# Kernel optimization log

Hardware: AMD Instinct MI355X
Metric: run time of the kernel (lower is better)

The kernel has to match this reference:

```python
import jax, jax.numpy as jnp
import numpy as np

N_NODES = 50000
N_EDGES = 1_600_000
IN_CH = 128
HIDDEN = 64
OUT_CH = 1


def glorot(key, shape):
    limit = np.sqrt(6.0 / (shape[0] + shape[1]))
    return jax.random.uniform(key, shape, jnp.float32, -limit, limit)


def setup_inputs() -> dict:
    key = jax.random.key(0)
    ks = jax.random.split(key, 6)
    x = jax.random.normal(ks[0], (N_NODES, IN_CH), jnp.float32)
    edge_index = jax.random.randint(ks[1], (2, N_EDGES), 0, N_NODES, jnp.int64)
    W1 = glorot(ks[2], (IN_CH, HIDDEN))
    b1 = jnp.zeros((HIDDEN,), jnp.float32)
    W2 = glorot(ks[3], (HIDDEN, HIDDEN // 2))
    b2 = jnp.zeros((HIDDEN // 2,), jnp.float32)
    Wh = glorot(ks[4], (HIDDEN // 2, OUT_CH))
    bh = jnp.zeros((OUT_CH,), jnp.float32)
    return {"x": x, "edge_index": edge_index, "W1": W1, "b1": b1,
            "W2": W2, "b2": b2, "Wh": Wh, "bh": bh}


def gcn_conv(x, src, dst, W, b):
    """PyG-style GCNConv: H' = D^{-1/2} (A + I) D^{-1/2} X W + b."""
    n = x.shape[0]
    h = x @ W  # transform first (smaller message dim)
    # degree of A + I (all edge weights = 1, self-loop weight = 1)
    deg = jax.ops.segment_sum(jnp.ones(src.shape[0], h.dtype), dst,
                              num_segments=n) + 1.0
    dinv = deg ** -0.5
    norm = dinv[src] * dinv[dst]                      # [E]
    msg = h[src] * norm[:, None]                      # [E, F] gather
    agg = jax.ops.segment_sum(msg, dst, num_segments=n)  # scatter-add
    agg = agg + h * (dinv * dinv)[:, None]            # self-loop term
    return agg + b


def reference(x, edge_index, W1, b1, W2, b2, Wh, bh):
    src, dst = edge_index[0], edge_index[1]
    h = jax.nn.relu(gcn_conv(x, src, dst, W1, b1))
    # dropout: inference mode (training=False) -> identity
    h = jax.nn.relu(gcn_conv(h, src, dst, W2, b2))
    return h @ Wh + bh
```

## Files before the change

kernel.cpp:

```cpp
#include <hip/hip_runtime.h>

#define N_NODES 50000
#define IN_CH 128
#define HID 64
#define HID2 32

constexpr int NB = 391;
constexpr int CHUNK = 4096;
constexpr int CAP = 5120;
#define FPSCALE 524288.0f
#define FPINV   0x1p-19f
#define T1SCALE 2048.0f
#define T1INV   0x1p-11f

__device__ __forceinline__ unsigned short f2bf(float f) {
    union { float f; unsigned u; } v; v.f = f;
    unsigned r = v.u + 0x7fff + ((v.u >> 16) & 1);
    return (unsigned short)(r >> 16);
}
__device__ __forceinline__ float bflo(unsigned d) {
    union { unsigned u; float f; } v; v.u = d << 16; return v.f;
}
__device__ __forceinline__ float bfhi(unsigned d) {
    union { unsigned u; float f; } v; v.u = d & 0xffff0000u; return v.f;
}
__device__ __forceinline__ unsigned pack16(int a, int b) {
    return ((unsigned)a & 0xffffu) | ((unsigned)b << 16);
}
__device__ __forceinline__ void acc2(int& a0, int& a1, unsigned u) {
    a0 += (int)(short)(u & 0xffffu);
    a1 += ((int)u) >> 16;
}

__global__ __launch_bounds__(1024) void bin_kernel(const int* __restrict__ src,
                                                   const int* __restrict__ dst,
                                                   int* __restrict__ bcur,
                                                   unsigned short* __restrict__ psrc,
                                                   unsigned char* __restrict__ pbyte, int E) {
    __shared__ int hist[NB], lbase[NB], gbase[NB], lcur[NB];
    __shared__ unsigned outp[CHUNK];
    __shared__ int wsum[16];
    int tid = threadIdx.x, lane = tid & 63;
    int base = blockIdx.x * CHUNK;
    int cnt = min(CHUNK, E - base);
    for (int i = tid; i < NB; i += 1024) hist[i] = 0;
    int es[CHUNK / 1024], ed[CHUNK / 1024];
    __syncthreads();
#pragma unroll
    for (int k = 0; k < CHUNK / 1024; k++) {
        int e = base + k * 1024 + tid;
        if (e < E) {
            es[k] = src[e];
            ed[k] = dst[e];
            atomicAdd(&hist[ed[k] >> 7], 1);
        }
    }
    __syncthreads();
    {
        int v = (tid < NB) ? hist[tid] : 0;
        int s = v;
#pragma unroll
        for (int d = 1; d < 64; d <<= 1) {
            int t = __shfl_up(s, d, 64);
            if (lane >= d) s += t;
        }
        if (lane == 63 && tid < 512) wsum[tid >> 6] = s;
        __syncthreads();
        if (tid == 0) {
            int run = 0;
#pragma unroll
            for (int w = 0; w < 8; w++) { int t = wsum[w]; wsum[w] = run; run += t; }
        }
        __syncthreads();
        if (tid < NB) lbase[tid] = wsum[tid >> 6] + s - v;
    }
    __syncthreads();
    for (int i = tid; i < NB; i += 1024) {
        gbase[i] = i * CAP + (hist[i] ? atomicAdd(&bcur[i], hist[i]) : 0);
        lcur[i] = lbase[i];
    }
    __syncthreads();
#pragma unroll
    for (int k = 0; k < CHUNK / 1024; k++) {
        int e = base + k * 1024 + tid;
        if (e < E) {
            int b = ed[k] >> 7;
            int p = atomicAdd(&lcur[b], 1);
            outp[p] = ((unsigned)es[k] << 16) | (unsigned)ed[k];
        }
    }
    __syncthreads();
#pragma unroll
    for (int k = 0; k < CHUNK / 1024; k++) {
        int i = k * 1024 + tid;
        if (i < cnt) {
            unsigned p = outp[i];
            int d = (int)(p & 0xffffu);
            int b = d >> 7;
            int gp = gbase[b] + (i - lbase[b]);
            psrc[gp] = (unsigned short)(p >> 16);
            pbyte[gp] = (unsigned char)(d & 127);
        }
    }
}

__global__ __launch_bounds__(1024) void fine_kernel(unsigned short* __restrict__ psrc,
                                                    const unsigned char* __restrict__ pbyte,
                                                    const int* __restrict__ bcur,
                                                    int* __restrict__ off,
                                                    unsigned short* __restrict__ len,
                                                    float* __restrict__ dinv, int N) {
    __shared__ unsigned short lsrc[CAP];
    __shared__ unsigned char lb[CAP];
    __shared__ int fh[128], fb[128], fc[128];
    __shared__ int wsum2[2];
    int b = blockIdx.x, tid = threadIdx.x, lane = tid & 63;
    int gb = b * CAP;
    int cnt = min(bcur[b], CAP);
    if (tid < 128) fh[tid] = 0;
    __syncthreads();
    for (int i = tid; i < cnt; i += 1024) {
        lsrc[i] = psrc[gb + i];
        int dl = pbyte[gb + i];
        lb[i] = (unsigned char)dl;
        atomicAdd(&fh[dl], 1);
    }
    __syncthreads();
    {
        int v = (tid < 128) ? fh[tid] : 0;
        int s = v;
#pragma unroll
        for (int d = 1; d < 64; d <<= 1) {
            int t = __shfl_up(s, d, 64);
            if (lane >= d) s += t;
        }
        if (lane == 63 && tid < 128) wsum2[tid >> 6] = s;
        __syncthreads();
        if (tid < 128) fb[tid] = ((tid >> 6) ? wsum2[0] : 0) + s - v;
    }
    __syncthreads();
    if (tid < 128) {
        fc[tid] = fb[tid];
        int node = (b << 7) + tid;
        if (node < N) {
            off[node] = gb + fb[tid];
            len[node] = (unsigned short)fh[tid];
            dinv[node] = rsqrtf((float)fh[tid] + 1.0f);
        }
    }
    __syncthreads();
    for (int i = tid; i < cnt; i += 1024) {
        int p = atomicAdd(&fc[lb[i]], 1);
        psrc[gb + p] = lsrc[i];
    }
}

template <int K, int J, int NPB>
__global__ __launch_bounds__(256) void gemm_s_kernel(const float* __restrict__ X,
                                                     const float* __restrict__ W,
                                                     const float* __restrict__ dinv,
                                                     short* __restrict__ out, int N) {
    constexpr int QJ = J / 4;
    constexpr int NPT = NPB / (256 / QJ);
    static_assert(NPT == 2, "layout assumes 2 nodes/thread");
    constexpr int RG = K / 4;
    constexpr int RS = K + 4;
    __shared__ float Ws[K * J];
    __shared__ float Xs[NPB * RS];
    int tid = threadIdx.x;
    if (blockIdx.x == 0 && tid < J / 2)
        ((unsigned*)(out + (size_t)N * J))[tid] = 0;
    for (int i = tid; i < K * J / 4; i += 256) ((float4*)Ws)[i] = ((const float4*)W)[i];
    int n0 = blockIdx.x * NPB;
    for (int i = tid; i < NPB * RG; i += 256) {
        int r = i / RG, c = i % RG;
        int n = n0 + r;
        float4 v = make_float4(0.f, 0.f, 0.f, 0.f);
        if (n < N) v = ((const float4*)(X + (size_t)n * K))[c];
        *(float4*)&Xs[r * RS + ((c ^ (r & 7)) << 2)] = v;
    }
    __syncthreads();
    int q = tid % QJ, g = (tid / QJ) * NPT;
    const float* xr0 = &Xs[g * RS];
    const float* xr1 = &Xs[(g + 1) * RS];
    int sw0 = g & 7, sw1 = (g + 1) & 7;
    float4 a0 = make_float4(0.f, 0.f, 0.f, 0.f);
    float4 a1 = make_float4(0.f, 0.f, 0.f, 0.f);
#pragma unroll 8
    for (int k = 0; k < K; k++) {
        float4 w = *(const float4*)&Ws[k * J + q * 4];
        float x0 = xr0[(((k >> 2) ^ sw0) << 2) + (k & 3)];
        float x1 = xr1[(((k >> 2) ^ sw1) << 2) + (k & 3)];
        a0.x += x0 * w.x; a0.y += x0 * w.y; a0.z += x0 * w.z; a0.w += x0 * w.w;
        a1.x += x1 * w.x; a1.y += x1 * w.y; a1.z += x1 * w.z; a1.w += x1 * w.w;
    }
#pragma unroll
    for (int t = 0; t < NPT; t++) {
        int n = n0 + g + t;
        if (n < N) {
            float4 a = t ? a1 : a0;
            float d0 = dinv[n] * T1SCALE;
            int v0 = max(-32767, min(32767, (int)lrintf(a.x * d0)));
            int v1 = max(-32767, min(32767, (int)lrintf(a.y * d0)));
            int v2 = max(-32767, min(32767, (int)lrintf(a.z * d0)));
            int v3 = max(-32767, min(32767, (int)lrintf(a.w * d0)));
            *(uint2*)(out + (size_t)n * J + q * 4) = make_uint2(pack16(v0, v1), pack16(v2, v3));
        }
    }
}

__global__ __launch_bounds__(256) void agg1_fused_kernel(const unsigned short* __restrict__ sorted_src,
                                                         const int* __restrict__ off,
                                                         const unsigned short* __restrict__ len,
                                                         const float* __restrict__ dinv,
                                                         const short* __restrict__ xtab,
                                                         const float* __restrict__ b1,
                                                         const float* __restrict__ W2,
                                                         unsigned short* __restrict__ hws, int N) {
    __shared__ float hrow[4][HID];
    int tid = threadIdx.x, wid = tid >> 6, lane = tid & 63;
    if (blockIdx.x == 0 && tid < HID2 / 2)
        ((unsigned*)(hws + (size_t)N * HID2))[tid] = 0;
    int n = blockIdx.x * 4 + wid;
    if (n >= N) return;
    int g = lane >> 3, fl = lane & 7;
    int start = off[n], len_ = len[n];
    float dvn = dinv[n];
    const unsigned* tb = (const unsigned*)xtab;
    const unsigned char* tbb = (const unsigned char*)xtab;
    int acc[8] = {0, 0, 0, 0, 0, 0, 0, 0};
    if (len_ <= 64) {
        int sall = (lane < len_) ? (int)sorted_src[start + lane] : N;
        unsigned fo = ((unsigned)fl) << 4;
        int nit = (len_ + 31) >> 5;
        for (int t = 0; t < nit; t++) {
            int eb = (t << 5) + g;
            int s0 = __shfl(sall, eb, 64);
            int s1 = __shfl(sall, eb + 8, 64);
            int s2 = __shfl(sall, eb + 16, 64);
            int s3 = __shfl(sall, eb + 24, 64);
            uint4 q0 = *(const uint4*)(tbb + ((((unsigned)s0) << 7) + fo));
            uint4 q1 = *(const uint4*)(tbb + ((((unsigned)s1) << 7) + fo));
            uint4 q2 = *(const uint4*)(tbb + ((((unsigned)s2) << 7) + fo));
            uint4 q3 = *(const uint4*)(tbb + ((((unsigned)s3) << 7) + fo));
            acc2(acc[0], acc[1], q0.x); acc2(acc[2], acc[3], q0.y);
            acc2(acc[4], acc[5], q0.z); acc2(acc[6], acc[7], q0.w);
            acc2(acc[0], acc[1], q1.x); acc2(acc[2], acc[3], q1.y);
            acc2(acc[4], acc[5], q1.z); acc2(acc[6], acc[7], q1.w);
            acc2(acc[0], acc[1], q2.x); acc2(acc[2], acc[3], q2.y);
            acc2(acc[4], acc[5], q2.z); acc2(acc[6], acc[7], q2.w);
            acc2(acc[0], acc[1], q3.x); acc2(acc[2], acc[3], q3.y);
            acc2(acc[4], acc[5], q3.z); acc2(acc[6], acc[7], q3.w);
        }
    } else {
        int i = start + g, end = start + len_;
        for (; i < end; i += 8) {
            int s = sorted_src[i];
            uint4 q = *(const uint4*)(tb + (size_t)s * 32 + fl * 4);
            acc2(acc[0], acc[1], q.x); acc2(acc[2], acc[3], q.y);
            acc2(acc[4], acc[5], q.z); acc2(acc[6], acc[7], q.w);
        }
    }
#pragma unroll
    for (int m = 8; m <= 32; m <<= 1)
#pragma unroll
        for (int j = 0; j < 8; j++) acc[j] += __shfl_xor(acc[j], m, 64);
    if (g == 0) {
        float dis = dvn * T1INV;
        uint4 q = *(const uint4*)(tb + (size_t)n * 32 + fl * 4);
        int sv[8];
        sv[0] = (int)(short)(q.x & 0xffffu); sv[1] = ((int)q.x) >> 16;
        sv[2] = (int)(short)(q.y & 0xffffu); sv[3] = ((int)q.y) >> 16;
        sv[4] = (int)(short)(q.z & 0xffffu); sv[5] = ((int)q.z) >> 16;
        sv[6] = (int)(short)(q.w & 0xffffu); sv[7] = ((int)q.w) >> 16;
        float4 bb0 = *(const float4*)(b1 + fl * 8);
        float4 bb1 = *(const float4*)(b1 + fl * 8 + 4);
        float bbv[8] = {bb0.x, bb0.y, bb0.z, bb0.w, bb1.x, bb1.y, bb1.z, bb1.w};
        float o[8];
#pragma unroll
        for (int j = 0; j < 8; j++)
            o[j] = fmaxf((float)(acc[j] + sv[j]) * dis + bbv[j], 0.f);
        *(float4*)&hrow[wid][fl * 8]     = make_float4(o[0], o[1], o[2], o[3]);
        *(float4*)&hrow[wid][fl * 8 + 4] = make_float4(o[4], o[5], o[6], o[7]);
    }
    int j = lane & 31, half = lane >> 5;
    const float* hb = &hrow[wid][half << 5];
    const float* w2b = W2 + ((half << 5) * HID2) + j;
    float p = 0.f;
#pragma unroll
    for (int k4 = 0; k4 < 8; k4++) {
        float4 h4 = *(const float4*)(hb + (k4 << 2));
        p += h4.x * w2b[(k4 * 4 + 0) * HID2];
        p += h4.y * w2b[(k4 * 4 + 1) * HID2];
        p += h4.z * w2b[(k4 * 4 + 2) * HID2];
        p += h4.w * w2b[(k4 * 4 + 3) * HID2];
    }
    p += __shfl_xor(p, 32, 64);
    if (lane < 32)
        hws[(size_t)n * HID2 + j] = f2bf(p * dvn * FPSCALE);
}

__global__ __launch_bounds__(256) void agg2_final_kernel(const unsigned short* __restrict__ sorted_src,
                                                         const int* __restrict__ off,
                                                         const unsigned short* __restrict__ len,
                                                         const float* __restrict__ dinv,
                                                         const unsigned short* __restrict__ hws,
                                                         const float* __restrict__ b2,
                                                         const float* __restrict__ Wh,
                                                         const float* __restrict__ bh,
                                                         float* __restrict__ out, int N) {
    int lane = threadIdx.x & 63;
    int n = blockIdx.x * 4 + (threadIdx.x >> 6);
    if (n >= N) return;
    int g = lane >> 2, fl = lane & 3;
    int start = off[n], len_ = len[n];
    const unsigned char* hbb = (const unsigned char*)hws;
    int acc[8] = {0, 0, 0, 0, 0, 0, 0, 0};
    if (len_ <= 64) {
        int sall = (lane < len_) ? (int)sorted_src[start + lane] : N;
        unsigned fo = ((unsigned)fl) << 4;
        int s0 = __shfl(sall, g, 64);
        int s1 = __shfl(sall, g + 16, 64);
        int s2 = __shfl(sall, g + 32, 64);
        int s3 = __shfl(sall, g + 48, 64);
        uint4 q0 = *(const uint4*)(hbb + ((((unsigned)s0) << 6) + fo));
        uint4 q1 = *(const uint4*)(hbb + ((((unsigned)s1) << 6) + fo));
        uint4 q2 = *(const uint4*)(hbb + ((((unsigned)s2) << 6) + fo));
        uint4 q3 = *(const uint4*)(hbb + ((((unsigned)s3) << 6) + fo));
        acc[0] += (int)bflo(q0.x) + (int)bflo(q1.x) + (int)bflo(q2.x) + (int)bflo(q3.x);
        acc[1] += (int)bfhi(q0.x) + (int)bfhi(q1.x) + (int)bfhi(q2.x) + (int)bfhi(q3.x);
        acc[2] += (int)bflo(q0.y) + (int)bflo(q1.y) + (int)bflo(q2.y) + (int)bflo(q3.y);
        acc[3] += (int)bfhi(q0.y) + (int)bfhi(q1.y) + (int)bfhi(q2.y) + (int)bfhi(q3.y);
        acc[4] += (int)bflo(q0.z) + (int)bflo(q1.z) + (int)bflo(q2.z) + (int)bflo(q3.z);
        acc[5] += (int)bfhi(q0.z) + (int)bfhi(q1.z) + (int)bfhi(q2.z) + (int)bfhi(q3.z);
        acc[6] += (int)bflo(q0.w) + (int)bflo(q1.w) + (int)bflo(q2.w) + (int)bflo(q3.w);
        acc[7] += (int)bfhi(q0.w) + (int)bfhi(q1.w) + (int)bfhi(q2.w) + (int)bfhi(q3.w);
    } else {
        int i = start + g, end = start + len_;
        for (; i < end; i += 16) {
            int s = sorted_src[i];
            uint4 q = *(const uint4*)(hws + (size_t)s * HID2 + fl * 8);
            acc[0] += (int)bflo(q.x); acc[1] += (int)bfhi(q.x);
            acc[2] += (int)bflo(q.y); acc[3] += (int)bfhi(q.y);
            acc[4] += (int)bflo(q.z); acc[5] += (int)bfhi(q.z);
            acc[6] += (int)bflo(q.w); acc[7] += (int)bfhi(q.w);
        }
    }
#pragma unroll
    for (int m = 4; m <= 32; m <<= 1)
#pragma unroll
        for (int j = 0; j < 8; j++) acc[j] += __shfl_xor(acc[j], m, 64);
    float dis = dinv[n] * FPINV;
    uint4 q = *(const uint4*)(hws + (size_t)n * HID2 + fl * 8);
    int sv[8] = {(int)bflo(q.x), (int)bfhi(q.x), (int)bflo(q.y), (int)bfhi(q.y),
                 (int)bflo(q.z), (int)bfhi(q.z), (int)bflo(q.w), (int)bfhi(q.w)};
    float4 bb0 = *(const float4*)(b2 + fl * 8);
    float4 bb1 = *(const float4*)(b2 + fl * 8 + 4);
    float bbv[8] = {bb0.x, bb0.y, bb0.z, bb0.w, bb1.x, bb1.y, bb1.z, bb1.w};
    float4 wv0 = *(const float4*)(Wh + fl * 8);
    float4 wv1 = *(const float4*)(Wh + fl * 8 + 4);
    float wvv[8] = {wv0.x, wv0.y, wv0.z, wv0.w, wv1.x, wv1.y, wv1.z, wv1.w};
    float p = 0.f;
#pragma unroll
    for (int j = 0; j < 8; j++)
        p += fmaxf((float)(acc[j] + sv[j]) * dis + bbv[j], 0.f) * wvv[j];
    p += __shfl_xor(p, 1, 64);
    p += __shfl_xor(p, 2, 64);
    if (lane == 0) out[n] = p + bh[0];
}

extern "C" void kernel_launch(void* const* d_in, const int* in_sizes, int n_in,
                              void* d_out, int out_size, void* d_ws, size_t ws_size,
                              hipStream_t stream) {
    const float* x  = (const float*)d_in[0];
    const int*   ei = (const int*)d_in[1];
    const float* W1 = (const float*)d_in[2];
    const float* b1 = (const float*)d_in[3];
    const float* W2 = (const float*)d_in[4];
    const float* b2 = (const float*)d_in[5];
    const float* Wh = (const float*)d_in[6];
    const float* bh = (const float*)d_in[7];
    float* out = (float*)d_out;

    const int N = N_NODES;
    const int E = in_sizes[1] / 2;
    const int* src = ei;
    const int* dst = ei + E;

    int* ws = (int*)d_ws;
    int*            bcur  = ws;
    int*            off   = bcur + 512;
    unsigned short* len   = (unsigned short*)(off + 50048);
    float*          dinv  = (float*)((int*)len + 25024);
    unsigned short* psrc  = (unsigned short*)(dinv + 50048);
    unsigned char*  pbyte = (unsigned char*)(psrc + (size_t)NB * CAP);
    short*          xtab  = (short*)(pbyte + (size_t)NB * CAP);
    unsigned short* hws   = (unsigned short*)(xtab + (size_t)(N + 1) * HID);

    hipMemsetAsync(bcur, 0, NB * sizeof(int), stream);

    int eblocks = (E + CHUNK - 1) / CHUNK;
    bin_kernel<<<eblocks, 1024, 0, stream>>>(src, dst, bcur, psrc, pbyte, E);
    fine_kernel<<<NB, 1024, 0, stream>>>(psrc, pbyte, bcur, off, len, dinv, N);

    gemm_s_kernel<IN_CH, HID, 32><<<(N + 31) / 32, 256, 0, stream>>>(x, W1, dinv, xtab, N);
    agg1_fused_kernel<<<(N + 3) / 4, 256, 0, stream>>>(psrc, off, len, dinv, xtab, b1, W2, hws, N);
    agg2_final_kernel<<<(N + 3) / 4, 256, 0, stream>>>(psrc, off, len, dinv, hws, b2, Wh, bh, out, N);
}
```

Measured before the change: 190.9 us.

## Pack node offset/length metadata, recompute dinv, use packed int16 adds in aggregation

Merges the per-node offset and length arrays into one uint2 metadata array and recomputes the degree normalisation from the length inside the aggregation kernels, so each node needs one load instead of three. The first-layer table is clamped to a narrower int16 range so pairs of rows can be summed with packed 16-bit adds without overflow. The small-degree aggregation loop is replaced by straight-line 32/64-edge paths. The second aggregation now accumulates in float instead of int. Risks are reduced precision headroom from the tighter clamp and more branchy code.

```diff
diff --git a/kernel.cpp b/kernel.cpp
--- a/kernel.cpp
+++ b/kernel.cpp
@@ -13,6 +13,8 @@
 #define T1SCALE 2048.0f
 #define T1INV   0x1p-11f
 
+typedef short short2e __attribute__((ext_vector_type(2)));
+
 __device__ __forceinline__ unsigned short f2bf(float f) {
     union { float f; unsigned u; } v; v.f = f;
     unsigned r = v.u + 0x7fff + ((v.u >> 16) & 1);
@@ -27,6 +29,17 @@
 __device__ __forceinline__ unsigned pack16(int a, int b) {
     return ((unsigned)a & 0xffffu) | ((unsigned)b << 16);
 }
+__device__ __forceinline__ unsigned pkadd(unsigned a, unsigned b) {
+    short2e x, y, r;
+    __builtin_memcpy(&x, &a, 4);
+    __builtin_memcpy(&y, &b, 4);
+    r = x + y;
+    unsigned d;
+    __builtin_memcpy(&d, &r, 4);
+    return d;
+}
+__device__ __forceinline__ int lo16(unsigned u) { return (int)(short)(u & 0xffffu); }
+__device__ __forceinline__ int hi16(unsigned u) { return ((int)u) >> 16; }
 __device__ __forceinline__ void acc2(int& a0, int& a1, unsigned u) {
     a0 += (int)(short)(u & 0xffffu);
     a1 += ((int)u) >> 16;
@@ -107,8 +120,7 @@
 __global__ __launch_bounds__(1024) void fine_kernel(unsigned short* __restrict__ psrc,
                                                     const unsigned char* __restrict__ pbyte,
                                                     const int* __restrict__ bcur,
-                                                    int* __restrict__ off,
-                                                    unsigned short* __restrict__ len,
+                                                    uint2* __restrict__ meta,
                                                     float* __restrict__ dinv, int N) {
     __shared__ unsigned short lsrc[CAP];
     __shared__ unsigned char lb[CAP];
@@ -143,8 +155,7 @@
         fc[tid] = fb[tid];
         int node = (b << 7) + tid;
         if (node < N) {
-            off[node] = gb + fb[tid];
-            len[node] = (unsigned short)fh[tid];
+            meta[node] = make_uint2((unsigned)(gb + fb[tid]), (unsigned)fh[tid]);
             dinv[node] = rsqrtf((float)fh[tid] + 1.0f);
         }
     }
@@ -200,19 +211,17 @@
         if (n < N) {
             float4 a = t ? a1 : a0;
             float d0 = dinv[n] * T1SCALE;
-            int v0 = max(-32767, min(32767, (int)lrintf(a.x * d0)));
-            int v1 = max(-32767, min(32767, (int)lrintf(a.y * d0)));
-            int v2 = max(-32767, min(32767, (int)lrintf(a.z * d0)));
-            int v3 = max(-32767, min(32767, (int)lrintf(a.w * d0)));
+            int v0 = max(-16383, min(16383, (int)lrintf(a.x * d0)));
+            int v1 = max(-16383, min(16383, (int)lrintf(a.y * d0)));
+            int v2 = max(-16383, min(16383, (int)lrintf(a.z * d0)));
+            int v3 = max(-16383, min(16383, (int)lrintf(a.w * d0)));
             *(uint2*)(out + (size_t)n * J + q * 4) = make_uint2(pack16(v0, v1), pack16(v2, v3));
         }
     }
 }
 
 __global__ __launch_bounds__(256) void agg1_fused_kernel(const unsigned short* __restrict__ sorted_src,
-                                                         const int* __restrict__ off,
-                                                         const unsigned short* __restrict__ len,
-                                                         const float* __restrict__ dinv,
+                                                         const uint2* __restrict__ meta,
                                                          const short* __restrict__ xtab,
                                                          const float* __restrict__ b1,
                                                          const float* __restrict__ W2,
@@ -224,33 +233,61 @@
     int n = blockIdx.x * 4 + wid;
     if (n >= N) return;
     int g = lane >> 3, fl = lane & 7;
-    int start = off[n], len_ = len[n];
-    float dvn = dinv[n];
+    uint2 mm = meta[n];
+    int start = (int)mm.x, len_ = (int)mm.y;
+    float dvn = rsqrtf((float)len_ + 1.0f);
     const unsigned* tb = (const unsigned*)xtab;
     const unsigned char* tbb = (const unsigned char*)xtab;
     int acc[8] = {0, 0, 0, 0, 0, 0, 0, 0};
     if (len_ <= 64) {
         int sall = (lane < len_) ? (int)sorted_src[start + lane] : N;
         unsigned fo = ((unsigned)fl) << 4;
-        int nit = (len_ + 31) >> 5;
-        for (int t = 0; t < nit; t++) {
-            int eb = (t << 5) + g;
-            int s0 = __shfl(sall, eb, 64);
-            int s1 = __shfl(sall, eb + 8, 64);
-            int s2 = __shfl(sall, eb + 16, 64);
-            int s3 = __shfl(sall, eb + 24, 64);
+        int s0 = __shfl(sall, g, 64);
+        int s1 = __shfl(sall, g + 8, 64);
+        int s2 = __shfl(sall, g + 16, 64);
+        int s3 = __shfl(sall, g + 24, 64);
+        if (len_ <= 32) {
             uint4 q0 = *(const uint4*)(tbb + ((((unsigned)s0) << 7) + fo));
             uint4 q1 = *(const uint4*)(tbb + ((((unsigned)s1) << 7) + fo));
             uint4 q2 = *(const uint4*)(tbb + ((((unsigned)s2) << 7) + fo));
             uint4 q3 = *(const uint4*)(tbb + ((((unsigned)s3) << 7) + fo));
-            acc2(acc[0], acc[1], q0.x); acc2(acc[2], acc[3], q0.y);
-            acc2(acc[4], acc[5], q0.z); acc2(acc[6], acc[7], q0.w);
-            acc2(acc[0], acc[1], q1.x); acc2(acc[2], acc[3], q1.y);
-            acc2(acc[4], acc[5], q1.z); acc2(acc[6], acc[7], q1.w);
-            acc2(acc[0], acc[1], q2.x); acc2(acc[2], acc[3], q2.y);
-            acc2(acc[4], acc[5], q2.z); acc2(acc[6], acc[7], q2.w);
-            acc2(acc[0], acc[1], q3.x); acc2(acc[2], acc[3], q3.y);
-            acc2(acc[4], acc[5], q3.z); acc2(acc[6], acc[7], q3.w);
+            unsigned pa0 = pkadd(q0.x, q1.x), pa1 = pkadd(q0.y, q1.y);
+            unsigned pa2 = pkadd(q0.z, q1.z), pa3 = pkadd(q0.w, q1.w);
+            unsigned pb0 = pkadd(q2.x, q3.x), pb1 = pkadd(q2.y, q3.y);
+            unsigned pb2 = pkadd(q2.z, q3.z), pb3 = pkadd(q2.w, q3.w);
+            acc[0] = lo16(pa0) + lo16(pb0); acc[1] = hi16(pa0) + hi16(pb0);
+            acc[2] = lo16(pa1) + lo16(pb1); acc[3] = hi16(pa1) + hi16(pb1);
+            acc[4] = lo16(pa2) + lo16(pb2); acc[5] = hi16(pa2) + hi16(pb2);
+            acc[6] = lo16(pa3) + lo16(pb3); acc[7] = hi16(pa3) + hi16(pb3);
+        } else {
+            int s4 = __shfl(sall, g + 32, 64);
+            int s5 = __shfl(sall, g + 40, 64);
+            int s6 = __shfl(sall, g + 48, 64);
+            int s7 = __shfl(sall, g + 56, 64);
+            uint4 q0 = *(const uint4*)(tbb + ((((unsigned)s0) << 7) + fo));
+            uint4 q1 = *(const uint4*)(tbb + ((((unsigned)s1) << 7) + fo));
+            uint4 q2 = *(const uint4*)(tbb + ((((unsigned)s2) << 7) + fo));
+            uint4 q3 = *(const uint4*)(tbb + ((((unsigned)s3) << 7) + fo));
+            uint4 q4 = *(const uint4*)(tbb + ((((unsigned)s4) << 7) + fo));
+            uint4 q5 = *(const uint4*)(tbb + ((((unsigned)s5) << 7) + fo));
+            uint4 q6 = *(const uint4*)(tbb + ((((unsigned)s6) << 7) + fo));
+            uint4 q7 = *(const uint4*)(tbb + ((((unsigned)s7) << 7) + fo));
+            unsigned pa0 = pkadd(q0.x, q1.x), pa1 = pkadd(q0.y, q1.y);
+            unsigned pa2 = pkadd(q0.z, q1.z), pa3 = pkadd(q0.w, q1.w);
+            unsigned pb0 = pkadd(q2.x, q3.x), pb1 = pkadd(q2.y, q3.y);
+            unsigned pb2 = pkadd(q2.z, q3.z), pb3 = pkadd(q2.w, q3.w);
+            unsigned pc0 = pkadd(q4.x, q5.x), pc1 = pkadd(q4.y, q5.y);
+            unsigned pc2 = pkadd(q4.z, q5.z), pc3 = pkadd(q4.w, q5.w);
+            unsigned pd0 = pkadd(q6.x, q7.x), pd1 = pkadd(q6.y, q7.y);
+            unsigned pd2 = pkadd(q6.z, q7.z), pd3 = pkadd(q6.w, q7.w);
+            acc[0] = (lo16(pa0) + lo16(pb0)) + (lo16(pc0) + lo16(pd0));
+            acc[1] = (hi16(pa0) + hi16(pb0)) + (hi16(pc0) + hi16(pd0));
+            acc[2] = (lo16(pa1) + lo16(pb1)) + (lo16(pc1) + lo16(pd1));
+            acc[3] = (hi16(pa1) + hi16(pb1)) + (hi16(pc1) + hi16(pd1));
+            acc[4] = (lo16(pa2) + lo16(pb2)) + (lo16(pc2) + lo16(pd2));
+            acc[5] = (hi16(pa2) + hi16(pb2)) + (hi16(pc2) + hi16(pd2));
+            acc[6] = (lo16(pa3) + lo16(pb3)) + (lo16(pc3) + lo16(pd3));
+            acc[7] = (hi16(pa3) + hi16(pb3)) + (hi16(pc3) + hi16(pd3));
         }
     } else {
         int i = start + g, end = start + len_;
@@ -301,9 +338,7 @@
 }
 
 __global__ __launch_bounds__(256) void agg2_final_kernel(const unsigned short* __restrict__ sorted_src,
-                                                         const int* __restrict__ off,
-                                                         const unsigned short* __restrict__ len,
-                                                         const float* __restrict__ dinv,
+                                                         const uint2* __restrict__ meta,
                                                          const unsigned short* __restrict__ hws,
                                                          const float* __restrict__ b2,
                                                          const float* __restrict__ Wh,
@@ -313,12 +348,14 @@
     int n = blockIdx.x * 4 + (threadIdx.x >> 6);
     if (n >= N) return;
     int g = lane >> 2, fl = lane & 3;
-    int start = off[n], len_ = len[n];
+    uint2 mm = meta[n];
+    int start = (int)mm.x, len_ = (int)mm.y;
+    float dvn = rsqrtf((float)len_ + 1.0f);
     const unsigned char* hbb = (const unsigned char*)hws;
-    int acc[8] = {0, 0, 0, 0, 0, 0, 0, 0};
+    float af[8] = {0.f, 0.f, 0.f, 0.f, 0.f, 0.f, 0.f, 0.f};
+    unsigned fo = ((unsigned)fl) << 4;
     if (len_ <= 64) {
         int sall = (lane < len_) ? (int)sorted_src[start + lane] : N;
-        unsigned fo = ((unsigned)fl) << 4;
         int s0 = __shfl(sall, g, 64);
         int s1 = __shfl(sall, g + 16, 64);
         int s2 = __shfl(sall, g + 32, 64);
@@ -327,33 +364,33 @@
         uint4 q1 = *(const uint4*)(hbb + ((((unsigned)s1) << 6) + fo));
         uint4 q2 = *(const uint4*)(hbb + ((((unsigned)s2) << 6) + fo));
         uint4 q3 = *(const uint4*)(hbb + ((((unsigned)s3) << 6) + fo));
-        acc[0] += (int)bflo(q0.x) + (int)bflo(q1.x) + (int)bflo(q2.x) + (int)bflo(q3.x);
-        acc[1] += (int)bfhi(q0.x) + (int)bfhi(q1.x) + (int)bfhi(q2.x) + (int)bfhi(q3.x);
-        acc[2] += (int)bflo(q0.y) + (int)bflo(q1.y) + (int)bflo(q2.y) + (int)bflo(q3.y);
-        acc[3] += (int)bfhi(q0.y) + (int)bfhi(q1.y) + (int)bfhi(q2.y) + (int)bfhi(q3.y);
-        acc[4] += (int)bflo(q0.z) + (int)bflo(q1.z) + (int)bflo(q2.z) + (int)bflo(q3.z);
-        acc[5] += (int)bfhi(q0.z) + (int)bfhi(q1.z) + (int)bfhi(q2.z) + (int)bfhi(q3.z);
-        acc[6] += (int)bflo(q0.w) + (int)bflo(q1.w) + (int)bflo(q2.w) + (int)bflo(q3.w);
-        acc[7] += (int)bfhi(q0.w) + (int)bfhi(q1.w) + (int)bfhi(q2.w) + (int)bfhi(q3.w);
+        af[0] = (bflo(q0.x) + bflo(q1.x)) + (bflo(q2.x) + bflo(q3.x));
+        af[1] = (bfhi(q0.x) + bfhi(q1.x)) + (bfhi(q2.x) + bfhi(q3.x));
+        af[2] = (bflo(q0.y) + bflo(q1.y)) + (bflo(q2.y) + bflo(q3.y));
+        af[3] = (bfhi(q0.y) + bfhi(q1.y)) + (bfhi(q2.y) + bfhi(q3.y));
+        af[4] = (bflo(q0.z) + bflo(q1.z)) + (bflo(q2.z) + bflo(q3.z));
+        af[5] = (bfhi(q0.z) + bfhi(q1.z)) + (bfhi(q2.z) + bfhi(q3.z));
+        af[6] = (bflo(q0.w) + bflo(q1.w)) + (bflo(q2.w) + bflo(q3.w));
+        af[7] = (bfhi(q0.w) + bfhi(q1.w)) + (bfhi(q2.w) + bfhi(q3.w));
     } else {
         int i = start + g, end = start + len_;
         for (; i < end; i += 16) {
             int s = sorted_src[i];
-            uint4 q = *(const uint4*)(hws + (size_t)s * HID2 + fl * 8);
-            acc[0] += (int)bflo(q.x); acc[1] += (int)bfhi(q.x);
-            acc[2] += (int)bflo(q.y); acc[3] += (int)bfhi(q.y);
-            acc[4] += (int)bflo(q.z); acc[5] += (int)bfhi(q.z);
-            acc[6] += (int)bflo(q.w); acc[7] += (int)bfhi(q.w);
+            uint4 q = *(const uint4*)(hbb + ((((unsigned)s) << 6) + fo));
+            af[0] += bflo(q.x); af[1] += bfhi(q.x);
+            af[2] += bflo(q.y); af[3] += bfhi(q.y);
+            af[4] += bflo(q.z); af[5] += bfhi(q.z);
+            af[6] += bflo(q.w); af[7] += bfhi(q.w);
         }
     }
 #pragma unroll
     for (int m = 4; m <= 32; m <<= 1)
 #pragma unroll
-        for (int j = 0; j < 8; j++) acc[j] += __shfl_xor(acc[j], m, 64);
-    float dis = dinv[n] * FPINV;
-    uint4 q = *(const uint4*)(hws + (size_t)n * HID2 + fl * 8);
-    int sv[8] = {(int)bflo(q.x), (int)bfhi(q.x), (int)bflo(q.y), (int)bfhi(q.y),
-                 (int)bflo(q.z), (int)bfhi(q.z), (int)bflo(q.w), (int)bfhi(q.w)};
+        for (int j = 0; j < 8; j++) af[j] += __shfl_xor(af[j], m, 64);
+    float dis = dvn * FPINV;
+    uint4 q = *(const uint4*)(hbb + ((((unsigned)n) << 6) + fo));
+    float sf[8] = {bflo(q.x), bfhi(q.x), bflo(q.y), bfhi(q.y),
+                   bflo(q.z), bfhi(q.z), bflo(q.w), bfhi(q.w)};
     float4 bb0 = *(const float4*)(b2 + fl * 8);
     float4 bb1 = *(const float4*)(b2 + fl * 8 + 4);
     float bbv[8] = {bb0.x, bb0.y, bb0.z, bb0.w, bb1.x, bb1.y, bb1.z, bb1.w};
@@ -363,7 +400,7 @@
     float p = 0.f;
 #pragma unroll
     for (int j = 0; j < 8; j++)
-        p += fmaxf((float)(acc[j] + sv[j]) * dis + bbv[j], 0.f) * wvv[j];
+        p += fmaxf((af[j] + sf[j]) * dis + bbv[j], 0.f) * wvv[j];
     p += __shfl_xor(p, 1, 64);
     p += __shfl_xor(p, 2, 64);
     if (lane == 0) out[n] = p + bh[0];
@@ -389,9 +426,8 @@
 
     int* ws = (int*)d_ws;
     int*            bcur  = ws;
-    int*            off   = bcur + 512;
-    unsigned short* len   = (unsigned short*)(off + 50048);
-    float*          dinv  = (float*)((int*)len + 25024);
+    uint2*          meta  = (uint2*)(bcur + 512);
+    float*          dinv  = (float*)(meta + 50048);
     unsigned short* psrc  = (unsigned short*)(dinv + 50048);
     unsigned char*  pbyte = (unsigned char*)(psrc + (size_t)NB * CAP);
     short*          xtab  = (short*)(pbyte + (size_t)NB * CAP);
@@ -401,9 +437,9 @@
 
     int eblocks = (E + CHUNK - 1) / CHUNK;
     bin_kernel<<<eblocks, 1024, 0, stream>>>(src, dst, bcur, psrc, pbyte, E);
-    fine_kernel<<<NB, 1024, 0, stream>>>(psrc, pbyte, bcur, off, len, dinv, N);
+    fine_kernel<<<NB, 1024, 0, stream>>>(psrc, pbyte, bcur, meta, dinv, N);
 
     gemm_s_kernel<IN_CH, HID, 32><<<(N + 31) / 32, 256, 0, stream>>>(x, W1, dinv, xtab, N);
-    agg1_fused_kernel<<<(N + 3) / 4, 256, 0, stream>>>(psrc, off, len, dinv, xtab, b1, W2, hws, N);
-    agg2_final_kernel<<<(N + 3) / 4, 256, 0, stream>>>(psrc, off, len, dinv, hws, b2, Wh, bh, out, N);
-}
+    agg1_fused_kernel<<<(N + 3) / 4, 256, 0, stream>>>(psrc, meta, xtab, b1, W2, hws, N);
+    agg2_final_kernel<<<(N + 3) / 4, 256, 0, stream>>>(psrc, meta, hws, b2, Wh, bh, out, N);
+}
```

Result: no change. 188.9 us (-1.1%).
